# Kernel optimization log

Hardware: AMD Instinct MI355X
Metric: run time of the kernel (lower is better)

Reference implementation:

```python
import jax, jax.numpy as jnp
import numpy as np

B = 64        # graphs
N0 = 2048     # nodes per graph
DEG = 16      # avg degree
IN = 128      # input_dim
H = 30        # hcs
NH = 11       # heads
OD = 8        # output_dim[i]
K1, K2, K3 = 1844, 1660, 1494  # ceil(0.9*n) chain


def setup_inputs() -> dict:
    key = jax.random.key(0)
    ks = jax.random.split(key, 32)
    N = B * N0
    E = N * DEG
    x = jax.random.normal(ks[0], (N, IN), jnp.float32)
    g = jnp.repeat(jnp.arange(B, dtype=jnp.int32), N0 * DEG)
    src = g * N0 + jax.random.randint(ks[1], (E,), 0, N0, dtype=jnp.int32)
    dst = g * N0 + jax.random.randint(ks[2], (E,), 0, N0, dtype=jnp.int32)
    edge_index = jnp.stack([src, dst])
    edge_attr = jax.random.uniform(ks[3], (E,), jnp.float32)
    batch = jnp.repeat(jnp.arange(B, dtype=jnp.int32), N0)
    s = 0.05
    def W(k, *shape):
        return jax.random.normal(k, shape, jnp.float32) * s
    return {
        'x': x, 'edge_index': edge_index, 'edge_attr': edge_attr, 'batch': batch,
        'ln_g': jnp.ones((IN,), jnp.float32), 'ln_b': jnp.zeros((IN,), jnp.float32),
        'W_rel1': W(ks[4], IN, H), 'b_rel1': W(ks[5], H), 'W_root1': W(ks[6], IN, H),
        'W_rel2': W(ks[7], H, H), 'b_rel2': W(ks[8], H), 'W_root2': W(ks[9], H, H),
        'W_rel3': W(ks[10], H, H), 'b_rel3': W(ks[11], H), 'W_root3': W(ks[12], H, H),
        'pool_w1': W(ks[13], H), 'pool_w2': W(ks[14], H), 'pool_w3': W(ks[15], H),
        'head_W1': W(ks[16], NH, 2 * H, 8 * H), 'head_b1': W(ks[17], NH, 8 * H),
        'head_W2': W(ks[18], NH, 8 * H, 32 * H), 'head_b2': W(ks[19], NH, 32 * H),
        'head_W3': W(ks[20], NH, 32 * H, OD), 'head_b3': W(ks[21], NH, OD),
    }


def _layernorm(x, g, b):
    m = x.mean(-1, keepdims=True)
    v = ((x - m) ** 2).mean(-1, keepdims=True)
    return (x - m) * jax.lax.rsqrt(v + 1e-5) * g + b


def _gconv(x, src, dst, ew, Wr, br, Ws, N):
    # PyG GraphConv: out = lin_rel(sum_j ew*x_j) + lin_root(x)
    agg = jax.ops.segment_sum(x[src] * ew[:, None], dst, num_segments=N)
    return agg @ Wr + br + x @ Ws


def _topk_pool(x, src, dst, ew, w, n, k):
    # score = tanh(x.w/||w||); keep top-k per graph; gate kept nodes by score
    score = jnp.tanh((x @ w) / jnp.linalg.norm(w)).reshape(B, n)
    vals, idx = jax.lax.top_k(score, k)                      # [B,k]
    xg = x.reshape(B, n, -1)
    xk = jnp.take_along_axis(xg, idx[:, :, None], axis=1) * vals[:, :, None]
    x_new = xk.reshape(B * k, -1)
    newidx = jnp.full((B, n), -1, jnp.int32)
    newidx = newidx.at[jnp.arange(B)[:, None], idx].set(
        jnp.broadcast_to(jnp.arange(k, dtype=jnp.int32), (B, k)))
    g = src // n
    ns = newidx[g, src % n]
    nd = newidx[g, dst % n]
    keep = (ns >= 0) & (nd >= 0)
    src_new = jnp.where(keep, g * k + ns, 0)
    dst_new = jnp.where(keep, g * k + nd, 0)
    ew_new = jnp.where(keep, ew, 0.0)
    return x_new, src_new, dst_new, ew_new


def _readout(x, k):
    xg = x.reshape(B, k, -1)
    return jnp.concatenate([xg.max(axis=1), xg.mean(axis=1)], axis=1)  # [B,2H]


def reference(x, edge_index, edge_attr, batch, ln_g, ln_b,
              W_rel1, b_rel1, W_root1, W_rel2, b_rel2, W_root2,
              W_rel3, b_rel3, W_root3, pool_w1, pool_w2, pool_w3,
              head_W1, head_b1, head_W2, head_b2, head_W3, head_b3):
    src, dst = edge_index[0], edge_index[1]
    ew = edge_attr
    h = _layernorm(x, ln_g, ln_b)

    h = jax.nn.relu(_gconv(h, src, dst, ew, W_rel1, b_rel1, W_root1, B * N0))
    h, src, dst, ew = _topk_pool(h, src, dst, ew, pool_w1, N0, K1)
    x1 = _readout(h, K1)

    h = jax.nn.relu(_gconv(h, src, dst, ew, W_rel2, b_rel2, W_root2, B * K1))
    h, src, dst, ew = _topk_pool(h, src, dst, ew, pool_w2, K1, K2)
    x2 = _readout(h, K2)

    h = jax.nn.relu(_gconv(h, src, dst, ew, W_rel3, b_rel3, W_root3, B * K2))
    h, src, dst, ew = _topk_pool(h, src, dst, ew, pool_w3, K2, K3)
    x3 = _readout(h, K3)

    z = jax.nn.relu(x1 + x2 + x3)                                   # [B,60]
    a = jax.nn.relu(jnp.einsum('bd,hdo->hbo', z, head_W1) + head_b1[:, None, :])
    a = jax.nn.relu(jnp.einsum('hbo,hop->hbp', a, head_W2) + head_b2[:, None, :])
    out = jnp.einsum('hbp,hpq->hbq', a, head_W3) + head_b3[:, None, :]
    return out  # [11, B, 8]
```

## Files before the change

kernel.cpp:

```cpp
#include <hip/hip_runtime.h>
#include <hip/hip_bf16.h>

#define B 64
#define N0 2048
#define DEG 16
#define IN_DIM 128
#define H 30
#define NH 11
#define K1 1844
#define K2 1660
#define K3 1494
#define NTOT (B * N0)
#define ETOT (NTOT * DEG)
#define EPG (ETOT / B)
#define RSTRIDE 32
#define ESTRIDE1 32768
#define ESTRIDE2 27648
#define RSEG 16

__global__ __launch_bounds__(256) void k_prep(
    const float* __restrict__ ln_g, const float* __restrict__ ln_b,
    const float* __restrict__ Wrel1, const float* __restrict__ brel1, const float* __restrict__ Wroot1,
    const float* __restrict__ Wrel2, const float* __restrict__ Wroot2,
    const float* __restrict__ Wrel3, const float* __restrict__ Wroot3,
    float* __restrict__ Wc1, float* __restrict__ S1, float* __restrict__ T1,
    float* __restrict__ Wc2, float* __restrict__ Wc3)
{
    int tid = threadIdx.x;
    for (int i = tid; i < IN_DIM * 60; i += 256) {
        int j = i / 60, c = i - j * 60;
        float w = (c < H) ? Wrel1[j * H + c] : Wroot1[j * H + (c - H)];
        Wc1[i] = w * ln_g[j];
    }
    if (tid < 60) {
        int c = tid;
        float s = 0.f, tt = 0.f;
        for (int j = 0; j < IN_DIM; ++j) {
            float w = (c < H) ? Wrel1[j * H + c] : Wroot1[j * H + (c - H)];
            s += w * ln_g[j];
            tt += w * ln_b[j];
        }
        S1[c] = s;
        T1[c] = (c < H) ? tt : tt + brel1[c - H];
    }
    for (int i = tid; i < H * 60; i += 256) {
        int j = i / 60, c = i - j * 60;
        Wc2[i] = (c < H) ? Wrel2[j * H + c] : Wroot2[j * H + (c - H)];
        Wc3[i] = (c < H) ? Wrel3[j * H + c] : Wroot3[j * H + (c - H)];
    }
}

__global__ __launch_bounds__(256) void k_lnproj(
    const float* __restrict__ x, const float* __restrict__ Wc,
    const float* __restrict__ S, const float* __restrict__ T,
    float* __restrict__ r, float* __restrict__ t)
{
    int row = blockIdx.x * 256 + threadIdx.x;
    const float* xr = x + (size_t)row * IN_DIM;
    float acc[60];
#pragma unroll
    for (int c = 0; c < 60; ++c) acc[c] = 0.f;
    float sum = 0.f, sumsq = 0.f;
    for (int jb = 0; jb < IN_DIM; jb += 8) {
        float4 a0 = *(const float4*)(xr + jb);
        float4 a1 = *(const float4*)(xr + jb + 4);
        float xs[8] = {a0.x, a0.y, a0.z, a0.w, a1.x, a1.y, a1.z, a1.w};
#pragma unroll
        for (int u = 0; u < 8; ++u) {
            float xv = xs[u];
            sum += xv;
            sumsq += xv * xv;
            const float* wrow = Wc + (jb + u) * 60;
#pragma unroll
            for (int c = 0; c < 60; ++c) acc[c] += xv * wrow[c];
        }
    }
    float mean = sum * (1.f / 128.f);
    float var = sumsq * (1.f / 128.f) - mean * mean;
    float rstd = 1.0f / sqrtf(var + 1e-5f);
    int rb = row * RSTRIDE, tb = row * H;
#pragma unroll
    for (int c = 0; c < H; ++c)
        r[rb + c] = rstd * (acc[c] - mean * S[c]) + T[c];
#pragma unroll
    for (int c = 0; c < H; ++c)
        t[tb + c] = rstd * (acc[30 + c] - mean * S[30 + c]) + T[30 + c];
}

__global__ __launch_bounds__(256) void k_proj30p(
    const float* __restrict__ hbuf, const int* __restrict__ sidx,
    const float* __restrict__ score, const float* __restrict__ Wc,
    const float* __restrict__ brel, float* __restrict__ r, float* __restrict__ t,
    int n_old, int k)
{
    int row = blockIdx.x * 256 + threadIdx.x;
    int g = row / k, j = row - g * k;
    int idx = sidx[g * k + j];
    float val = score[g * n_old + idx];
    const float* hr = hbuf + (size_t)(g * n_old + idx) * RSTRIDE;
    float hv[32];
#pragma unroll
    for (int m = 0; m < 8; ++m) {
        float4 q = *(const float4*)(hr + m * 4);
        hv[m * 4] = q.x; hv[m * 4 + 1] = q.y; hv[m * 4 + 2] = q.z; hv[m * 4 + 3] = q.w;
    }
    float acc[60];
#pragma unroll
    for (int c = 0; c < 60; ++c) acc[c] = 0.f;
    for (int m = 0; m < H; ++m) {
        const float* wrow = Wc + m * 60;
        float xv = hv[m];
#pragma unroll
        for (int c = 0; c < 60; ++c) acc[c] += xv * wrow[c];
    }
    int rb = row * RSTRIDE, tb = row * H;
#pragma unroll
    for (int c = 0; c < H; ++c) r[rb + c] = val * acc[c];
#pragma unroll
    for (int c = 0; c < H; ++c) t[tb + c] = val * acc[30 + c] + brel[c];
}

__global__ __launch_bounds__(1024) void k_hist1(
    const int* __restrict__ dst, unsigned short* __restrict__ rank,
    int* __restrict__ chunkCnt)
{
    __shared__ unsigned int cnt[2048];
    int chunk = blockIdx.x, g = chunk >> 2;
    for (int i = threadIdx.x; i < 2048; i += 1024) cnt[i] = 0;
    __syncthreads();
    int e0 = chunk * 8192;
#pragma unroll
    for (int u = 0; u < 8; ++u) {
        int e = e0 + u * 1024 + threadIdx.x;
        int d = dst[e] - g * N0;
        rank[e] = (unsigned short)atomicAdd(&cnt[d], 1u);
    }
    __syncthreads();
    for (int i = threadIdx.x; i < 2048; i += 1024) chunkCnt[chunk * 2048 + i] = cnt[i];
}

__global__ __launch_bounds__(1024) void k_scat1(
    const int* __restrict__ src, const int* __restrict__ dst, const float* __restrict__ ew,
    const unsigned short* __restrict__ rank, const int* __restrict__ chunkOff,
    float2* __restrict__ sOut)
{
    int chunk = blockIdx.x, g = chunk >> 2;
    int e0 = chunk * 8192;
#pragma unroll
    for (int u = 0; u < 8; ++u) {
        int e = e0 + u * 1024 + threadIdx.x;
        int d = dst[e] - g * N0;
        int pos = chunkOff[chunk * 2048 + d] + (int)rank[e];
        sOut[(size_t)g * ESTRIDE1 + pos] = make_float2(__int_as_float(src[e]), ew[e]);
    }
}

__global__ __launch_bounds__(1024) void k_histE(
    const int* __restrict__ src0, const int* __restrict__ dst0,
    const int* __restrict__ mapc, unsigned short* __restrict__ rank,
    int* __restrict__ chunkCnt)
{
    __shared__ unsigned int cnt[2048];
    int chunk = blockIdx.x;
    for (int i = threadIdx.x; i < 2048; i += 1024) cnt[i] = 0;
    __syncthreads();
    int e0 = chunk * 8192;
#pragma unroll
    for (int u = 0; u < 8; ++u) {
        int e = e0 + u * 1024 + threadIdx.x;
        int dd = mapc[dst0[e]];
        int ss = mapc[src0[e]];
        if (dd >= 0 && ss >= 0)
            rank[e] = (unsigned short)atomicAdd(&cnt[dd], 1u);
    }
    __syncthreads();
    for (int i = threadIdx.x; i < 2048; i += 1024) chunkCnt[chunk * 2048 + i] = cnt[i];
}

__global__ __launch_bounds__(1024) void k_scatE(
    const int* __restrict__ src0, const int* __restrict__ dst0,
    const float* __restrict__ ew, const int* __restrict__ mapc,
    const unsigned short* __restrict__ rank, const int* __restrict__ chunkOff,
    float2* __restrict__ sOut, int k_new, int estride)
{
    int chunk = blockIdx.x, g = chunk >> 2;
    int e0 = chunk * 8192;
#pragma unroll
    for (int u = 0; u < 8; ++u) {
        int e = e0 + u * 1024 + threadIdx.x;
        int dd = mapc[dst0[e]];
        int ss = mapc[src0[e]];
        if (dd >= 0 && ss >= 0) {
            int pos = chunkOff[chunk * 2048 + dd] + (int)rank[e];
            sOut[(size_t)g * estride + pos] =
                make_float2(__int_as_float(g * k_new + ss), ew[e]);
        }
    }
}

__global__ __launch_bounds__(1024) void k_scan(
    int* __restrict__ chunkCnt, int* __restrict__ runStart, int* __restrict__ runLen)
{
    __shared__ int bufA[2048], bufB[2048];
    int g = blockIdx.x;
    int c0[2], c1[2], c2[2], tt[2];
    for (int h2 = 0; h2 < 2; ++h2) {
        int d = threadIdx.x + h2 * 1024;
        c0[h2] = chunkCnt[(g * 4 + 0) * 2048 + d];
        c1[h2] = chunkCnt[(g * 4 + 1) * 2048 + d];
        c2[h2] = chunkCnt[(g * 4 + 2) * 2048 + d];
        int c3 = chunkCnt[(g * 4 + 3) * 2048 + d];
        tt[h2] = c0[h2] + c1[h2] + c2[h2] + c3;
        bufA[d] = tt[h2];
    }
    __syncthreads();
    int* s_ = bufA; int* d_ = bufB;
    for (int off = 1; off < 2048; off <<= 1) {
        for (int h2 = 0; h2 < 2; ++h2) {
            int d = threadIdx.x + h2 * 1024;
            int v = s_[d];
            if (d >= off) v += s_[d - off];
            d_[d] = v;
        }
        __syncthreads();
        int* tmp = s_; s_ = d_; d_ = tmp;
    }
    for (int h2 = 0; h2 < 2; ++h2) {
        int d = threadIdx.x + h2 * 1024;
        int ex = s_[d] - tt[h2];
        runStart[g * 2048 + d] = ex;
        runLen[g * 2048 + d] = tt[h2];
        chunkCnt[(g * 4 + 0) * 2048 + d] = ex;
        chunkCnt[(g * 4 + 1) * 2048 + d] = ex + c0[h2];
        chunkCnt[(g * 4 + 2) * 2048 + d] = ex + c0[h2] + c1[h2];
        chunkCnt[(g * 4 + 3) * 2048 + d] = ex + c0[h2] + c1[h2] + c2[h2];
    }
}

__global__ __launch_bounds__(256) void k_gather(
    const float2* __restrict__ sE, const int* __restrict__ runS, const int* __restrict__ runL,
    const float* __restrict__ rp, const float* __restrict__ t, float* __restrict__ h,
    const float* __restrict__ poolw, float* __restrict__ score,
    int n, int estride, int nblocks)
{
    int b = blockIdx.x;
    int cpx = nblocks >> 3;
    b = (b & 7) * cpx + (b >> 3);
    int slot = threadIdx.x >> 5, j = threadIdx.x & 31;
    int v = b * 8 + slot;
    int g = v / n;
    int local = v - g * n;
    int s0 = runS[g * 2048 + local], len = runL[g * 2048 + local];
    const float2* meta = sE + (size_t)g * estride + s0;
    float acc = 0.f;
    for (int c = 0; c < len; c += 8) {
        int lim = len - c; if (lim > 8) lim = 8;
        float2 m[8];
#pragma unroll
        for (int u = 0; u < 8; ++u) m[u] = meta[c + (u < lim ? u : 0)];
#pragma unroll
        for (int u = 0; u < 8; ++u) {
            int s = __float_as_int(m[u].x);
            float w = (u < lim) ? m[u].y : 0.f;
            acc += rp[(size_t)s * RSTRIDE + j] * w;
        }
    }
    float wj = (j < H) ? poolw[j] : 0.f;
    float hval = 0.f;
    if (j < H) {
        hval = fmaxf(acc + t[v * H + j], 0.f);
        h[(size_t)v * RSTRIDE + j] = hval;
    }
    float p = hval * wj, q = wj * wj;
#pragma unroll
    for (int off = 16; off > 0; off >>= 1) {
        p += __shfl_xor(p, off, 32);
        q += __shfl_xor(q, off, 32);
    }
    if (j == 0) score[v] = tanhf(p / sqrtf(q));
}

__global__ __launch_bounds__(1024) void k_topk_map(
    const float* __restrict__ score, int* __restrict__ sidx, int* __restrict__ mapc,
    int n, int k, int first)
{
    __shared__ unsigned long long keys[2048];
    __shared__ int inv[2048];
    int g = blockIdx.x;
    for (int i = threadIdx.x; i < 2048; i += 1024) {
        unsigned long long key = ~0ull;
        if (i < n) {
            float s = score[g * n + i];
            if (s == 0.f) s = 0.f;
            unsigned u = __float_as_uint(s);
            unsigned asc = (u & 0x80000000u) ? ~u : (u | 0x80000000u);
            unsigned desc = ~asc;
            key = ((unsigned long long)desc << 32) | (unsigned)i;
        }
        keys[i] = key;
        inv[i] = -1;
    }
    __syncthreads();
    for (int kk = 2; kk <= 2048; kk <<= 1) {
        for (int jj = kk >> 1; jj > 0; jj >>= 1) {
            for (int i = threadIdx.x; i < 2048; i += 1024) {
                int ixj = i ^ jj;
                if (ixj > i) {
                    unsigned long long a = keys[i], bb = keys[ixj];
                    bool up = ((i & kk) == 0);
                    if ((a > bb) == up) { keys[i] = bb; keys[ixj] = a; }
                }
            }
            __syncthreads();
        }
    }
    for (int j = threadIdx.x; j < k; j += 1024) {
        int idx = (int)(keys[j] & 0xffffffffu);
        sidx[g * k + j] = idx;
        inv[idx] = j;
    }
    __syncthreads();
    if (first) {
        for (int v = threadIdx.x; v < N0; v += 1024)
            mapc[g * N0 + v] = inv[v];
    } else {
        for (int v = threadIdx.x; v < N0; v += 1024) {
            int m = mapc[g * N0 + v];
            mapc[g * N0 + v] = (m >= 0) ? inv[m] : -1;
        }
    }
}

__global__ __launch_bounds__(256) void k_rpart(
    const float* __restrict__ hbuf, const int* __restrict__ sidx,
    const float* __restrict__ score, float* __restrict__ pmax, float* __restrict__ psum,
    int n_old, int k)
{
    __shared__ float smax[8][32], ssum[8][32];
    int g = blockIdx.y, seg = blockIdx.x;
    int clen = (k + RSEG - 1) / RSEG;
    int start = seg * clen;
    int end = start + clen; if (end > k) end = k;
    int f = threadIdx.x & 31, rr = threadIdx.x >> 5;
    float mx = -INFINITY, sm = 0.f;
    if (f < H) {
        for (int j = start + rr; j < end; j += 8) {
            int idx = sidx[g * k + j];
            float val = score[g * n_old + idx];
            float v = hbuf[(size_t)(g * n_old + idx) * RSTRIDE + f] * val;
            mx = fmaxf(mx, v);
            sm += v;
        }
    }
    smax[rr][f] = mx; ssum[rr][f] = sm;
    __syncthreads();
    if (rr == 0) {
        for (int q = 1; q < 8; ++q) { mx = fmaxf(mx, smax[q][f]); sm += ssum[q][f]; }
        pmax[(g * RSEG + seg) * 32 + f] = mx;
        psum[(g * RSEG + seg) * 32 + f] = sm;
    }
}

__global__ __launch_bounds__(64) void k_zfin(
    const float* __restrict__ pm1, const float* __restrict__ ps1,
    const float* __restrict__ pm2, const float* __restrict__ ps2,
    const float* __restrict__ pm3, const float* __restrict__ ps3,
    float* __restrict__ z)
{
    int g = blockIdx.x, c = threadIdx.x;
    if (c >= 60) return;
    float v1, v2, v3;
    if (c < H) {
        float m1 = -INFINITY, m2 = -INFINITY, m3 = -INFINITY;
        for (int s = 0; s < RSEG; ++s) {
            m1 = fmaxf(m1, pm1[(g * RSEG + s) * 32 + c]);
            m2 = fmaxf(m2, pm2[(g * RSEG + s) * 32 + c]);
            m3 = fmaxf(m3, pm3[(g * RSEG + s) * 32 + c]);
        }
        v1 = m1; v2 = m2; v3 = m3;
    } else {
        int f = c - H;
        float s1 = 0.f, s2 = 0.f, s3 = 0.f;
        for (int s = 0; s < RSEG; ++s) {
            s1 += ps1[(g * RSEG + s) * 32 + f];
            s2 += ps2[(g * RSEG + s) * 32 + f];
            s3 += ps3[(g * RSEG + s) * 32 + f];
        }
        v1 = s1 / (float)K1; v2 = s2 / (float)K2; v3 = s3 / (float)K3;
    }
    z[g * 60 + c] = fmaxf(v1 + v2 + v3, 0.f);
}

__global__ __launch_bounds__(256) void k_mlp1(
    const float* __restrict__ z, const float* __restrict__ W,
    const float* __restrict__ bias, float* __restrict__ a)
{
    int hb = blockIdx.x, hh = hb >> 6, b = hb & 63;
    __shared__ float zr[60];
    if (threadIdx.x < 60) zr[threadIdx.x] = z[b * 60 + threadIdx.x];
    __syncthreads();
    int o = threadIdx.x;
    if (o < 240) {
        float acc = bias[hh * 240 + o];
        const float* Wp = W + hh * 60 * 240;
#pragma unroll
        for (int d = 0; d < 60; ++d) acc += zr[d] * Wp[d * 240 + o];
        a[(hh * B + b) * 240 + o] = fmaxf(acc, 0.f);
    }
}

__global__ __launch_bounds__(320) void k_mlp2(
    const float* __restrict__ a1, const float* __restrict__ W,
    const float* __restrict__ bias, float* __restrict__ a2)
{
    int hh = blockIdx.x >> 3;
    int bb = (blockIdx.x & 7) * 8;
    __shared__ float ar[8][240];
    for (int i = threadIdx.x; i < 8 * 240; i += 320) {
        int rr = i / 240, o = i - rr * 240;
        ar[rr][o] = a1[(hh * B + bb + rr) * 240 + o];
    }
    __syncthreads();
    const float* Wp = W + hh * 240 * 960;
    float accv[3][8];
#pragma unroll
    for (int q = 0; q < 3; ++q)
#pragma unroll
        for (int rr = 0; rr < 8; ++rr) accv[q][rr] = 0.f;
#pragma unroll 2
    for (int o = 0; o < 240; ++o) {
        float w0 = Wp[o * 960 + threadIdx.x];
        float w1 = Wp[o * 960 + threadIdx.x + 320];
        float w2 = Wp[o * 960 + threadIdx.x + 640];
#pragma unroll
        for (int rr = 0; rr < 8; ++rr) {
            float av = ar[rr][o];
            accv[0][rr] += w0 * av;
            accv[1][rr] += w1 * av;
            accv[2][rr] += w2 * av;
        }
    }
#pragma unroll
    for (int q = 0; q < 3; ++q) {
        int p = threadIdx.x + q * 320;
        float bv = bias[hh * 960 + p];
#pragma unroll
        for (int rr = 0; rr < 8; ++rr)
            a2[(hh * B + bb + rr) * 960 + p] = fmaxf(accv[q][rr] + bv, 0.f);
    }
}

__global__ __launch_bounds__(64) void k_mlp3(
    const float* __restrict__ a2, const float* __restrict__ W,
    const float* __restrict__ bias, float* __restrict__ out)
{
    int hb = blockIdx.x, hh = hb >> 6, b = hb & 63;
    __shared__ float ar[960];
    __shared__ float part[64];
    for (int i = threadIdx.x; i < 960; i += 64) ar[i] = a2[(hh * B + b) * 960 + i];
    __syncthreads();
    int q = threadIdx.x & 7, c = threadIdx.x >> 3;
    const float* Wp = W + hh * 960 * 8;
    float acc = 0.f;
    for (int p = c; p < 960; p += 8) acc += ar[p] * Wp[p * 8 + q];
    part[threadIdx.x] = acc;
    __syncthreads();
    if (threadIdx.x < 8) {
        float s = bias[hh * 8 + threadIdx.x];
        for (int cc = 0; cc < 8; ++cc) s += part[cc * 8 + threadIdx.x];
        out[(hh * B + b) * 8 + threadIdx.x] = s;
    }
}

extern "C" void kernel_launch(void* const* d_in, const int* in_sizes, int n_in,
                              void* d_out, int out_size, void* d_ws, size_t ws_size,
                              hipStream_t stream)
{
    const float* x       = (const float*)d_in[0];
    const int*   eidx    = (const int*)d_in[1];
    const int*   src0    = eidx;
    const int*   dst0    = eidx + ETOT;
    const float* ew0     = (const float*)d_in[2];
    const float* ln_g    = (const float*)d_in[4];
    const float* ln_b    = (const float*)d_in[5];
    const float* W_rel1  = (const float*)d_in[6];
    const float* b_rel1  = (const float*)d_in[7];
    const float* W_root1 = (const float*)d_in[8];
    const float* W_rel2  = (const float*)d_in[9];
    const float* b_rel2  = (const float*)d_in[10];
    const float* W_root2 = (const float*)d_in[11];
    const float* W_rel3  = (const float*)d_in[12];
    const float* b_rel3  = (const float*)d_in[13];
    const float* W_root3 = (const float*)d_in[14];
    const float* pool_w1 = (const float*)d_in[15];
    const float* pool_w2 = (const float*)d_in[16];
    const float* pool_w3 = (const float*)d_in[17];
    const float* head_W1 = (const float*)d_in[18];
    const float* head_b1 = (const float*)d_in[19];
    const float* head_W2 = (const float*)d_in[20];
    const float* head_b2 = (const float*)d_in[21];
    const float* head_W3 = (const float*)d_in[22];
    const float* head_b3 = (const float*)d_in[23];

    float* ws     = (float*)d_ws;
    float* rbuf   = ws;
    float* tbuf   = rbuf + (size_t)NTOT * RSTRIDE;
    float* abuf   = tbuf + (size_t)NTOT * H;
    float2* sA    = (float2*)(abuf + (size_t)NTOT * RSTRIDE);
    float2* sB    = sA + (size_t)B * ESTRIDE1;
    float* score  = (float*)(sB + (size_t)B * ESTRIDE2);
    int*   sidx   = (int*)(score + NTOT);
    int*   mapc   = sidx + NTOT;
    int*   runSA  = mapc + NTOT;
    int*   runLA  = runSA + B * 2048;
    int*   runSB  = runLA + B * 2048;
    int*   runLB  = runSB + B * 2048;
    float* pm1    = (float*)(runLB + B * 2048);
    float* ps1    = pm1 + B * RSEG * 32;
    float* pm2    = ps1 + B * RSEG * 32;
    float* ps2    = pm2 + B * RSEG * 32;
    float* pm3    = ps2 + B * RSEG * 32;
    float* ps3    = pm3 + B * RSEG * 32;
    float* zb     = ps3 + B * RSEG * 32;
    float* Wc1    = zb + B * 60;
    float* S1     = Wc1 + IN_DIM * 60;
    float* T1     = S1 + 60;
    float* Wc2    = T1 + 60;
    float* Wc3    = Wc2 + H * 60;
    int* chunkBuf         = (int*)abuf;
    unsigned short* rank  = (unsigned short*)((char*)abuf + (4u << 20));
    float* a1 = rbuf;
    float* a2 = a1 + NH * B * 240;

    k_prep<<<1, 256, 0, stream>>>(ln_g, ln_b, W_rel1, b_rel1, W_root1,
                                  W_rel2, W_root2, W_rel3, W_root3,
                                  Wc1, S1, T1, Wc2, Wc3);

    k_hist1<<<256, 1024, 0, stream>>>(dst0, rank, chunkBuf);
    k_scan<<<B, 1024, 0, stream>>>(chunkBuf, runSA, runLA);
    k_scat1<<<256, 1024, 0, stream>>>(src0, dst0, ew0, rank, chunkBuf, sA);
    k_lnproj<<<NTOT / 256, 256, 0, stream>>>(x, Wc1, S1, T1, rbuf, tbuf);
    k_gather<<<NTOT / 8, 256, 0, stream>>>(sA, runSA, runLA, rbuf, tbuf, abuf,
                                           pool_w1, score, N0, ESTRIDE1, NTOT / 8);
    k_topk_map<<<B, 1024, 0, stream>>>(score, sidx, mapc, N0, K1, 1);
    k_rpart<<<dim3(RSEG, B), 256, 0, stream>>>(abuf, sidx, score, pm1, ps1, N0, K1);
    k_proj30p<<<B * K1 / 256, 256, 0, stream>>>(abuf, sidx, score, Wc2, b_rel2,
                                                rbuf, tbuf, N0, K1);

    k_histE<<<256, 1024, 0, stream>>>(src0, dst0, mapc, rank, chunkBuf);
    k_scan<<<B, 1024, 0, stream>>>(chunkBuf, runSB, runLB);
    k_scatE<<<256, 1024, 0, stream>>>(src0, dst0, ew0, mapc, rank, chunkBuf, sB,
                                      K1, ESTRIDE2);
    k_gather<<<B * K1 / 8, 256, 0, stream>>>(sB, runSB, runLB, rbuf, tbuf, abuf,
                                             pool_w2, score, K1, ESTRIDE2, B * K1 / 8);
    k_topk_map<<<B, 1024, 0, stream>>>(score, sidx, mapc, K1, K2, 0);
    k_rpart<<<dim3(RSEG, B), 256, 0, stream>>>(abuf, sidx, score, pm2, ps2, K1, K2);
    k_proj30p<<<B * K2 / 256, 256, 0, stream>>>(abuf, sidx, score, Wc3, b_rel3,
                                                rbuf, tbuf, K1, K2);

    k_histE<<<256, 1024, 0, stream>>>(src0, dst0, mapc, rank, chunkBuf);
    k_scan<<<B, 1024, 0, stream>>>(chunkBuf, runSA, runLA);
    k_scatE<<<256, 1024, 0, stream>>>(src0, dst0, ew0, mapc, rank, chunkBuf, sA,
                                      K2, ESTRIDE1);
    k_gather<<<B * K2 / 8, 256, 0, stream>>>(sA, runSA, runLA, rbuf, tbuf, abuf,
                                             pool_w3, score, K2, ESTRIDE1, B * K2 / 8);
    k_topk_map<<<B, 1024, 0, stream>>>(score, sidx, mapc, K2, K3, 0);
    k_rpart<<<dim3(RSEG, B), 256, 0, stream>>>(abuf, sidx, score, pm3, ps3, K2, K3);

    k_zfin<<<B, 64, 0, stream>>>(pm1, ps1, pm2, ps2, pm3, ps3, zb);
    k_mlp1<<<NH * B, 256, 0, stream>>>(zb, head_W1, head_b1, a1);
    k_mlp2<<<NH * 8, 320, 0, stream>>>(a1, head_W2, head_b2, a2);
    k_mlp3<<<NH * B, 64, 0, stream>>>(a2, head_W3, head_b3, (float*)d_out);
}
```

Baseline: 577.2 us.

## Stage projection weights in LDS, pad t to stride 32, retile head MLP2

k_lnproj and k_proj30p now copy the combined projection weights into shared memory and read them as float4. They also write r and t rows as padded float4 stores, with t moved to a 32-float stride. The gather kernel and the workspace layout are updated to match. k_mlp2 is retiled to 165 blocks that each hold all 64 batch rows of one head in LDS and compute a 64-column slice, with 16 rows per thread. This targets uniform global weight loads, scalar stores and low block count in the head MLP, at the cost of a larger LDS footprint (30KB in lnproj, 60KB in mlp2).

```diff
diff --git a/kernel.cpp b/kernel.cpp
--- a/kernel.cpp
+++ b/kernel.cpp
@@ -55,36 +55,63 @@
     const float* __restrict__ S, const float* __restrict__ T,
     float* __restrict__ r, float* __restrict__ t)
 {
+    __shared__ float wlds[IN_DIM * 60];
+    for (int i = threadIdx.x; i < IN_DIM * 60 / 4; i += 256)
+        ((float4*)wlds)[i] = ((const float4*)Wc)[i];
+    __syncthreads();
     int row = blockIdx.x * 256 + threadIdx.x;
-    const float* xr = x + (size_t)row * IN_DIM;
+    const float4* xr4 = (const float4*)(x + (size_t)row * IN_DIM);
     float acc[60];
 #pragma unroll
     for (int c = 0; c < 60; ++c) acc[c] = 0.f;
     float sum = 0.f, sumsq = 0.f;
-    for (int jb = 0; jb < IN_DIM; jb += 8) {
-        float4 a0 = *(const float4*)(xr + jb);
-        float4 a1 = *(const float4*)(xr + jb + 4);
-        float xs[8] = {a0.x, a0.y, a0.z, a0.w, a1.x, a1.y, a1.z, a1.w};
+    float4 qa = xr4[0], qb = xr4[1];
+    for (int jb = 0; jb < 16; ++jb) {
+        float xs[8] = {qa.x, qa.y, qa.z, qa.w, qb.x, qb.y, qb.z, qb.w};
+        if (jb < 15) { qa = xr4[jb * 2 + 2]; qb = xr4[jb * 2 + 3]; }
 #pragma unroll
         for (int u = 0; u < 8; ++u) {
             float xv = xs[u];
-            sum += xv;
-            sumsq += xv * xv;
-            const float* wrow = Wc + (jb + u) * 60;
-#pragma unroll
-            for (int c = 0; c < 60; ++c) acc[c] += xv * wrow[c];
+            sum += xv; sumsq += xv * xv;
+            const float4* w4 = (const float4*)&wlds[(jb * 8 + u) * 60];
+#pragma unroll
+            for (int c4 = 0; c4 < 15; ++c4) {
+                float4 wv = w4[c4];
+                acc[c4 * 4 + 0] += xv * wv.x;
+                acc[c4 * 4 + 1] += xv * wv.y;
+                acc[c4 * 4 + 2] += xv * wv.z;
+                acc[c4 * 4 + 3] += xv * wv.w;
+            }
         }
     }
     float mean = sum * (1.f / 128.f);
     float var = sumsq * (1.f / 128.f) - mean * mean;
     float rstd = 1.0f / sqrtf(var + 1e-5f);
-    int rb = row * RSTRIDE, tb = row * H;
-#pragma unroll
-    for (int c = 0; c < H; ++c)
-        r[rb + c] = rstd * (acc[c] - mean * S[c]) + T[c];
-#pragma unroll
-    for (int c = 0; c < H; ++c)
-        t[tb + c] = rstd * (acc[30 + c] - mean * S[30 + c]) + T[30 + c];
+    float4* rr4 = (float4*)(r + (size_t)row * RSTRIDE);
+    float4* tt4 = (float4*)(t + (size_t)row * RSTRIDE);
+#pragma unroll
+    for (int q4 = 0; q4 < 7; ++q4) {
+        float4 rv, tv;
+        rv.x = rstd * (acc[q4 * 4 + 0] - mean * S[q4 * 4 + 0]) + T[q4 * 4 + 0];
+        rv.y = rstd * (acc[q4 * 4 + 1] - mean * S[q4 * 4 + 1]) + T[q4 * 4 + 1];
+        rv.z = rstd * (acc[q4 * 4 + 2] - mean * S[q4 * 4 + 2]) + T[q4 * 4 + 2];
+        rv.w = rstd * (acc[q4 * 4 + 3] - mean * S[q4 * 4 + 3]) + T[q4 * 4 + 3];
+        tv.x = rstd * (acc[30 + q4 * 4 + 0] - mean * S[30 + q4 * 4 + 0]) + T[30 + q4 * 4 + 0];
+        tv.y = rstd * (acc[30 + q4 * 4 + 1] - mean * S[30 + q4 * 4 + 1]) + T[30 + q4 * 4 + 1];
+        tv.z = rstd * (acc[30 + q4 * 4 + 2] - mean * S[30 + q4 * 4 + 2]) + T[30 + q4 * 4 + 2];
+        tv.w = rstd * (acc[30 + q4 * 4 + 3] - mean * S[30 + q4 * 4 + 3]) + T[30 + q4 * 4 + 3];
+        rr4[q4] = rv; tt4[q4] = tv;
+    }
+    {
+        float4 rv, tv;
+        rv.x = rstd * (acc[28] - mean * S[28]) + T[28];
+        rv.y = rstd * (acc[29] - mean * S[29]) + T[29];
+        rv.z = 0.f; rv.w = 0.f;
+        tv.x = rstd * (acc[58] - mean * S[58]) + T[58];
+        tv.y = rstd * (acc[59] - mean * S[59]) + T[59];
+        tv.z = 0.f; tv.w = 0.f;
+        rr4[7] = rv; tt4[7] = tv;
+    }
 }
 
 __global__ __launch_bounds__(256) void k_proj30p(
@@ -93,31 +120,66 @@
     const float* __restrict__ brel, float* __restrict__ r, float* __restrict__ t,
     int n_old, int k)
 {
+    __shared__ float wlds[H * 60];
+    for (int i = threadIdx.x; i < H * 60 / 4; i += 256)
+        ((float4*)wlds)[i] = ((const float4*)Wc)[i];
+    __syncthreads();
     int row = blockIdx.x * 256 + threadIdx.x;
     int g = row / k, j = row - g * k;
     int idx = sidx[g * k + j];
     float val = score[g * n_old + idx];
     const float* hr = hbuf + (size_t)(g * n_old + idx) * RSTRIDE;
-    float hv[32];
-#pragma unroll
-    for (int m = 0; m < 8; ++m) {
-        float4 q = *(const float4*)(hr + m * 4);
-        hv[m * 4] = q.x; hv[m * 4 + 1] = q.y; hv[m * 4 + 2] = q.z; hv[m * 4 + 3] = q.w;
-    }
+    const float4* hr4 = (const float4*)hr;
     float acc[60];
 #pragma unroll
     for (int c = 0; c < 60; ++c) acc[c] = 0.f;
-    for (int m = 0; m < H; ++m) {
-        const float* wrow = Wc + m * 60;
-        float xv = hv[m];
-#pragma unroll
-        for (int c = 0; c < 60; ++c) acc[c] += xv * wrow[c];
-    }
-    int rb = row * RSTRIDE, tb = row * H;
-#pragma unroll
-    for (int c = 0; c < H; ++c) r[rb + c] = val * acc[c];
-#pragma unroll
-    for (int c = 0; c < H; ++c) t[tb + c] = val * acc[30 + c] + brel[c];
+    auto body = [&](int m, float xv) {
+        const float4* w4 = (const float4*)&wlds[m * 60];
+#pragma unroll
+        for (int c4 = 0; c4 < 15; ++c4) {
+            float4 wv = w4[c4];
+            acc[c4 * 4 + 0] += xv * wv.x;
+            acc[c4 * 4 + 1] += xv * wv.y;
+            acc[c4 * 4 + 2] += xv * wv.z;
+            acc[c4 * 4 + 3] += xv * wv.w;
+        }
+    };
+#pragma unroll
+    for (int mb = 0; mb < 7; ++mb) {
+        float4 hq = hr4[mb];
+        body(mb * 4 + 0, hq.x);
+        body(mb * 4 + 1, hq.y);
+        body(mb * 4 + 2, hq.z);
+        body(mb * 4 + 3, hq.w);
+    }
+    {
+        float2 h2 = *(const float2*)(hr + 28);
+        body(28, h2.x);
+        body(29, h2.y);
+    }
+    float4* rr4 = (float4*)(r + (size_t)row * RSTRIDE);
+    float4* tt4 = (float4*)(t + (size_t)row * RSTRIDE);
+#pragma unroll
+    for (int q4 = 0; q4 < 7; ++q4) {
+        float4 rv, tv;
+        rv.x = val * acc[q4 * 4 + 0];
+        rv.y = val * acc[q4 * 4 + 1];
+        rv.z = val * acc[q4 * 4 + 2];
+        rv.w = val * acc[q4 * 4 + 3];
+        tv.x = val * acc[30 + q4 * 4 + 0] + brel[q4 * 4 + 0];
+        tv.y = val * acc[30 + q4 * 4 + 1] + brel[q4 * 4 + 1];
+        tv.z = val * acc[30 + q4 * 4 + 2] + brel[q4 * 4 + 2];
+        tv.w = val * acc[30 + q4 * 4 + 3] + brel[q4 * 4 + 3];
+        rr4[q4] = rv; tt4[q4] = tv;
+    }
+    {
+        float4 rv, tv;
+        rv.x = val * acc[28]; rv.y = val * acc[29]; rv.z = 0.f; rv.w = 0.f;
+        tv.x = val * acc[58] + brel[28];
+        tv.y = val * acc[59] + brel[29];
+        tv.z = 0.f; tv.w = 0.f;
+        rr4[7] = rv; tt4[7] = tv;
+    }
 }
 
 __global__ __launch_bounds__(1024) void k_hist1(
@@ -268,7 +330,7 @@
     float wj = (j < H) ? poolw[j] : 0.f;
     float hval = 0.f;
     if (j < H) {
-        hval = fmaxf(acc + t[v * H + j], 0.f);
+        hval = fmaxf(acc + t[(size_t)v * RSTRIDE + j], 0.f);
         h[(size_t)v * RSTRIDE + j] = hval;
     }
     float p = hval * wj, q = wj * wj;
@@ -409,45 +471,34 @@
     }
 }
 
-__global__ __launch_bounds__(320) void k_mlp2(
+__global__ __launch_bounds__(256) void k_mlp2(
     const float* __restrict__ a1, const float* __restrict__ W,
     const float* __restrict__ bias, float* __restrict__ a2)
 {
-    int hh = blockIdx.x >> 3;
-    int bb = (blockIdx.x & 7) * 8;
-    __shared__ float ar[8][240];
-    for (int i = threadIdx.x; i < 8 * 240; i += 320) {
-        int rr = i / 240, o = i - rr * 240;
-        ar[rr][o] = a1[(hh * B + bb + rr) * 240 + o];
-    }
-    __syncthreads();
-    const float* Wp = W + hh * 240 * 960;
-    float accv[3][8];
-#pragma unroll
-    for (int q = 0; q < 3; ++q)
-#pragma unroll
-        for (int rr = 0; rr < 8; ++rr) accv[q][rr] = 0.f;
-#pragma unroll 2
+    __shared__ float a1t[64 * 240];
+    int hh = blockIdx.x / 15, ct = blockIdx.x % 15;
+    const float4* ag = (const float4*)(a1 + (size_t)hh * B * 240);
+    for (int i = threadIdx.x; i < 64 * 240 / 4; i += 256)
+        ((float4*)a1t)[i] = ag[i];
+    __syncthreads();
+    int col = threadIdx.x & 63, rg = threadIdx.x >> 6;
+    const float* Wp = W + (size_t)hh * 240 * 960 + ct * 64 + col;
+    float acc[16];
+#pragma unroll
+    for (int i = 0; i < 16; ++i) acc[i] = 0.f;
+#pragma unroll 4
     for (int o = 0; o < 240; ++o) {
-        float w0 = Wp[o * 960 + threadIdx.x];
-        float w1 = Wp[o * 960 + threadIdx.x + 320];
-        float w2 = Wp[o * 960 + threadIdx.x + 640];
-#pragma unroll
-        for (int rr = 0; rr < 8; ++rr) {
-            float av = ar[rr][o];
-            accv[0][rr] += w0 * av;
-            accv[1][rr] += w1 * av;
-            accv[2][rr] += w2 * av;
-        }
-    }
-#pragma unroll
-    for (int q = 0; q < 3; ++q) {
-        int p = threadIdx.x + q * 320;
-        float bv = bias[hh * 960 + p];
-#pragma unroll
-        for (int rr = 0; rr < 8; ++rr)
-            a2[(hh * B + bb + rr) * 960 + p] = fmaxf(accv[q][rr] + bv, 0.f);
-    }
+        float w = Wp[(size_t)o * 960];
+        const float* ar = &a1t[0];
+#pragma unroll
+        for (int i = 0; i < 16; ++i)
+            acc[i] += w * ar[(rg * 16 + i) * 240 + o];
+    }
+    float bv = bias[hh * 960 + ct * 64 + col];
+#pragma unroll
+    for (int i = 0; i < 16; ++i)
+        a2[((size_t)hh * B + rg * 16 + i) * 960 + ct * 64 + col] =
+            fmaxf(acc[i] + bv, 0.f);
 }
 
 __global__ __launch_bounds__(64) void k_mlp3(
@@ -505,7 +556,7 @@
     float* ws     = (float*)d_ws;
     float* rbuf   = ws;
     float* tbuf   = rbuf + (size_t)NTOT * RSTRIDE;
-    float* abuf   = tbuf + (size_t)NTOT * H;
+    float* abuf   = tbuf + (size_t)NTOT * RSTRIDE;
     float2* sA    = (float2*)(abuf + (size_t)NTOT * RSTRIDE);
     float2* sB    = sA + (size_t)B * ESTRIDE1;
     float* score  = (float*)(sB + (size_t)B * ESTRIDE2);
@@ -569,6 +620,6 @@
 
     k_zfin<<<B, 64, 0, stream>>>(pm1, ps1, pm2, ps2, pm3, ps3, zb);
     k_mlp1<<<NH * B, 256, 0, stream>>>(zb, head_W1, head_b1, a1);
-    k_mlp2<<<NH * 8, 320, 0, stream>>>(a1, head_W2, head_b2, a2);
+    k_mlp2<<<NH * 15, 256, 0, stream>>>(a1, head_W2, head_b2, a2);
     k_mlp3<<<NH * B, 64, 0, stream>>>(a2, head_W3, head_b3, (float*)d_out);
 }
```

Measured after the change: 557.2 us. 3.5% less time.
